# Kernel optimization log

Hardware: AMD Instinct MI355X
Metric: run time of the kernel (lower is better)

Reference implementation:

```python
import jax, jax.numpy as jnp
import numpy as np

BS, L, D = 64, 100, 512
ITEM_NUM = 100000
N = BS * (L + 1)  # number of in-batch candidate items
MASK_VAL = -10000.0


def setup_inputs() -> dict:
    key = jax.random.key(0)
    ks = jax.random.split(key, 8)
    sample_items_id = jax.random.randint(ks[0], (BS, L + 1), 1, ITEM_NUM + 1, dtype=jnp.int32)
    log_mask = jax.random.randint(ks[1], (BS, L), 0, 2, dtype=jnp.int32)
    pop_prob = jax.random.uniform(ks[2], (ITEM_NUM + 1,), minval=1e-3, maxval=1.0, dtype=jnp.float32)
    id_emb = jax.random.normal(ks[3], (ITEM_NUM + 1, D), dtype=jnp.float32) * 0.02
    scale = 1.0 / np.sqrt(D)
    W_ih = jax.random.normal(ks[4], (D, 3 * D), dtype=jnp.float32) * scale
    W_hh = jax.random.normal(ks[5], (D, 3 * D), dtype=jnp.float32) * scale
    b_ih = jnp.zeros((3 * D,), jnp.float32)
    b_hh = jnp.zeros((3 * D,), jnp.float32)
    return dict(sample_items_id=sample_items_id, log_mask=log_mask, pop_prob=pop_prob,
                id_emb=id_emb, W_ih=W_ih, W_hh=W_hh, b_ih=b_ih, b_hh=b_hh)


def gru_forward(x, W_ih, W_hh, b_ih, b_hh):
    # x: (B, T, D) -> per-step hidden states (B, T, D)  (GRU4Rec user encoder)
    B, T, Dh = x.shape
    gates_x = jnp.einsum('btd,de->bte', x, W_ih) + b_ih  # precompute input gates (B,T,3D)

    def step(h, gx):
        gh = h @ W_hh + b_hh
        xr, xz, xn = jnp.split(gx, 3, axis=-1)
        hr, hz, hn = jnp.split(gh, 3, axis=-1)
        r = jax.nn.sigmoid(xr + hr)
        z = jax.nn.sigmoid(xz + hz)
        n = jnp.tanh(xn + r * hn)
        h_new = (1.0 - z) * n + z * h
        return h_new, h_new

    h0 = jnp.zeros((B, Dh), x.dtype)
    _, hs = jax.lax.scan(step, h0, jnp.swapaxes(gates_x, 0, 1))  # (T,B,D)
    return jnp.swapaxes(hs, 0, 1)


def reference(sample_items_id, log_mask, pop_prob, id_emb, W_ih, W_hh, b_ih, b_hh):
    ids_flat = sample_items_id.reshape(-1)                 # (N,)
    debias = jnp.log(pop_prob[ids_flat])                   # (N,) debias_logits
    score_embs = id_emb[ids_flat]                          # (N, D)
    input_embs = score_embs.reshape(BS, L + 1, D)
    prec = gru_forward(input_embs[:, :-1, :], W_ih, W_hh, b_ih, b_hh)  # (BS, L, D)
    prec_vec = prec.reshape(BS * L, D)

    logits = prec_vec @ score_embs.T - debias[None, :]     # (BS*L, N)
    # mask padded candidate columns: cat(log_mask, ones(bs,1)) flattened == 0
    col_valid = jnp.concatenate([log_mask, jnp.ones((BS, 1), log_mask.dtype)], axis=1).reshape(-1)
    logits = jnp.where(col_valid[None, :] == 0, MASK_VAL, logits)
    logits = logits.reshape(BS, L, N)

    # per-sample negative exclusion: column k is rejected for sample i if
    # ids_flat[k] appears anywhere in sample i's own item list
    reject = (ids_flat[None, None, :] == sample_items_id[:, :, None]).any(axis=1)  # (BS, N)
    mask3 = jnp.broadcast_to(reject[:, None, :], (BS, L, N))
    # keep the ground-truth target position (i, j, i*(L+1)+j+1) unmasked
    tgt = jnp.arange(BS)[:, None] * (L + 1) + jnp.arange(L)[None, :] + 1  # (BS, L)
    col = jnp.arange(N)[None, None, :]
    mask3 = mask3 & (col != tgt[:, :, None])
    logits = jnp.where(mask3, MASK_VAL, logits)

    logits = logits.reshape(BS * L, N)
    labels = tgt.reshape(-1)
    logp = jax.nn.log_softmax(logits, axis=-1)
    nll = -jnp.take_along_axis(logp, labels[:, None], axis=1)[:, 0]
    w = (log_mask.reshape(-1) != 0).astype(logits.dtype)
    loss = jnp.sum(nll * w) / jnp.maximum(jnp.sum(w), 1.0)
    return loss
```

## Files before the change

### kernel.cpp

```cpp
#include <hip/hip_runtime.h>
#include <hip/hip_bf16.h>

#define BSZ   64
#define SEQL  100
#define DIM   512
#define L1P   101
#define NCOLS 6464
#define NROWS 6400
#define D3    1536
#define MASKV -10000.0f
#define M0    16.0f

#define SGRP  4
#define SPG   16
#define DBLK  16
#define DPB   32
#define GRU_BLOCKS (SGRP * DBLK)
#define SENT64 0x7FC07FC07FC07FC0ULL
#define INIT_N  409600
#define INIT_NP 410624

typedef __attribute__((ext_vector_type(8))) short bf16x8;
typedef __attribute__((ext_vector_type(4))) float f32x4;

__device__ __forceinline__ float sigm(float x)  { return 1.f / (1.f + __expf(-x)); }
__device__ __forceinline__ float ftanh(float x) { float e = __expf(2.f * x); return 1.f - 2.f / (e + 1.f); }
__device__ __forceinline__ ushort f2bf(float x) {
    __hip_bfloat16 b = __float2bfloat16(x);
    return *(ushort*)&b;
}

__global__ void init_ws(float* s_glob, float* acc, uint4* prec_all)
{
    int t = blockIdx.x * 256 + threadIdx.x;
    if (t < INIT_N) {
        uint4 s; s.x = 0x7FC07FC0u; s.y = 0x7FC07FC0u; s.z = 0x7FC07FC0u; s.w = 0x7FC07FC0u;
        prec_all[t] = s;
    } else if (t < INIT_NP) {
        uint4 z; z.x = 0u; z.y = 0u; z.z = 0u; z.w = 0u;
        prec_all[t] = z;
    }
    if (t < NROWS) s_glob[t] = 0.f;
    if (t < 2) acc[t] = 0.f;
}

__global__ void gather_embs(const int* __restrict__ ids, const float* __restrict__ emb,
                            ushort* __restrict__ score16)
{
    int idx = blockIdx.x * 256 + threadIdx.x;
    int row = idx >> 7, c4 = idx & 127;
    int id = ids[row];
    float4 v = *(const float4*)&emb[(size_t)id * DIM + c4 * 4];
    ushort4 u;
    u.x = f2bf(v.x); u.y = f2bf(v.y); u.z = f2bf(v.z); u.w = f2bf(v.w);
    *(ushort4*)&score16[(size_t)row * DIM + c4 * 4] = u;
}

__global__ void aux_kernel(const int* __restrict__ ids, const float* __restrict__ pop,
                           const int* __restrict__ lmask,
                           float* __restrict__ debias, int* __restrict__ colv)
{
    int k = blockIdx.x * 256 + threadIdx.x;
    if (k >= NCOLS) return;
    int id = ids[k];
    debias[k] = __logf(pop[id]);
    int j = k % L1P;
    colv[k] = (j == SEQL) ? 1 : lmask[(k / L1P) * SEQL + j];
}

__global__ void build_reject(const int* __restrict__ ids, const int* __restrict__ colv,
                             unsigned char* __restrict__ rejm)
{
    __shared__ int s_ids[L1P];
    int i = blockIdx.y;
    int tid = threadIdx.x;
    if (tid < L1P) s_ids[tid] = ids[i * L1P + tid];
    __syncthreads();
    int k = blockIdx.x * 256 + tid;
    if (k >= NCOLS) return;
    int myid = ids[k];
    int rej = 0;
    for (int j = 0; j < L1P; ++j) rej |= (myid == s_ids[j]);
    unsigned char code = (colv[k] == 0) ? 1 : (rej ? 2 : 0);
    rejm[(size_t)i * NCOLS + k] = code;
}

__global__ __launch_bounds__(256) void wt_tile(const float* __restrict__ W,
                                               ushort* __restrict__ WT)
{
    __shared__ float tile[64][65];
    int c0 = blockIdx.x * 64, k0 = blockIdx.y * 64;
    int tx = threadIdx.x & 63, ty = threadIdx.x >> 6;
    for (int r = ty; r < 64; r += 4)
        tile[r][tx] = W[(size_t)(k0 + r) * D3 + c0 + tx];
    __syncthreads();
    for (int r = ty; r < 64; r += 4)
        WT[(size_t)(c0 + r) * DIM + k0 + tx] = f2bf(tile[tx][r]);
}

__global__ __launch_bounds__(256) void gates_mfma(
    const ushort* __restrict__ score16, const ushort* __restrict__ WIT,
    const float* __restrict__ b_ih, float* __restrict__ gates)
{
    int n0 = blockIdx.x * 64, r0 = blockIdx.y * 64;
    int tid = threadIdx.x;
    int w = tid >> 6, lane = tid & 63, l15 = lane & 15, quad = lane >> 4;
    int r = r0 + w * 16 + l15;
    int i = r / SEQL, j = r % SEQL;
    const ushort* ap = score16 + (size_t)(i * L1P + j) * DIM + quad * 8;
    bf16x8 af[16];
#pragma unroll
    for (int c = 0; c < 16; ++c) af[c] = *(const bf16x8*)(ap + c * 32);

    f32x4 acc[4] = {{0,0,0,0},{0,0,0,0},{0,0,0,0},{0,0,0,0}};
#pragma unroll
    for (int c = 0; c < 16; ++c) {
#pragma unroll
        for (int nt = 0; nt < 4; ++nt) {
            const ushort* bp = WIT + (size_t)(n0 + nt * 16 + l15) * DIM + quad * 8 + c * 32;
            bf16x8 bb = *(const bf16x8*)bp;
            acc[nt] = __builtin_amdgcn_mfma_f32_16x16x32_bf16(af[c], bb, acc[nt], 0, 0, 0);
        }
    }
#pragma unroll
    for (int nt = 0; nt < 4; ++nt) {
        int n = n0 + nt * 16 + l15;
        float bi = b_ih[n];
#pragma unroll
        for (int p = 0; p < 4; ++p) {
            int rr = r0 + w * 16 + quad * 4 + p;
            gates[(size_t)rr * D3 + n] = acc[nt][p] + bi;
        }
    }
}

__global__ __launch_bounds__(256) void gru_mfma(
    const ushort* __restrict__ WT,
    const float* __restrict__ b_hh,
    const float* __restrict__ gates,
    ushort* __restrict__ prec16)
{
    __shared__ float  red[2][3][256];
    __shared__ ushort hpub[16][32];

    int b = blockIdx.x;
    int sg = b >> 4, db = b & 15;
    int s0 = sg * SPG, d0 = db * DPB;
    int tid = threadIdx.x;
    int w = tid >> 6, lane = tid & 63, l15 = lane & 15, quad = lane >> 4;
    int wc = w & 1, wk = w >> 1;
    int kb = wk * 8;

    bf16x8 wreg[3][8];
#pragma unroll
    for (int g = 0; g < 3; ++g)
#pragma unroll
        for (int cc = 0; cc < 8; ++cc)
            wreg[g][cc] = *(const bf16x8*)(WT
                + (size_t)(g * 512 + d0 + wc * 16 + l15) * DIM
                + (kb + cc) * 32 + quad * 8);

    int d = d0 + wc * 16 + l15;
    float bhr = b_hh[d], bhz = b_hh[512 + d], bhn = b_hh[1024 + d];
    float hprev[4] = {0.f, 0.f, 0.f, 0.f};

    for (int t = 0; t < SEQL; ++t) {
        float xr[4], xz[4], xn[4];
        if (wk == 0) {
#pragma unroll
            for (int p = 0; p < 4; ++p) {
                int ss = s0 + quad * 4 + p;
                const float* gx = gates + ((size_t)ss * SEQL + t) * D3;
                xr[p] = gx[d]; xz[p] = gx[512 + d]; xn[p] = gx[1024 + d];
            }
        }
        f32x4 acc[3] = {{0,0,0,0},{0,0,0,0},{0,0,0,0}};
        if (t > 0) {
            const ushort* ap = prec16
                + ((size_t)(s0 + l15) * SEQL + (t - 1)) * DIM + quad * 8;
            unsigned long long v[16];
            bool again = true;
            while (again) {
#pragma unroll
                for (int u = 0; u < 16; ++u) {
                    const unsigned long long* p64 = (const unsigned long long*)
                        (ap + (kb + (u >> 1)) * 32 + (u & 1) * 4);
                    v[u] = __hip_atomic_load(p64, __ATOMIC_RELAXED,
                                             __HIP_MEMORY_SCOPE_AGENT);
                }
                unsigned long long bad = 0ull;
#pragma unroll
                for (int u = 0; u < 16; ++u) {
                    unsigned long long x = v[u] ^ SENT64;
                    bad |= (x - 0x0001000100010001ULL) & ~x & 0x8000800080008000ULL;
                }
                again = (bad != 0ull);
                if (again) __builtin_amdgcn_s_sleep(1);
            }
#pragma unroll
            for (int cc = 0; cc < 8; ++cc) {
                union { unsigned long long q[2]; bf16x8 h; } af;
                af.q[0] = v[2 * cc]; af.q[1] = v[2 * cc + 1];
#pragma unroll
                for (int g = 0; g < 3; ++g)
                    acc[g] = __builtin_amdgcn_mfma_f32_16x16x32_bf16(
                        af.h, wreg[g][cc], acc[g], 0, 0, 0);
            }
        }
        if (wk == 1) {
#pragma unroll
            for (int g = 0; g < 3; ++g)
                *(f32x4*)&red[wc][g][lane * 4] = acc[g];
        }
        __syncthreads();
        if (wk == 0) {
#pragma unroll
            for (int p = 0; p < 4; ++p) {
                float a0 = acc[0][p] + red[wc][0][lane * 4 + p];
                float a1 = acc[1][p] + red[wc][1][lane * 4 + p];
                float a2 = acc[2][p] + red[wc][2][lane * 4 + p];
                float r = sigm(xr[p] + a0 + bhr);
                float z = sigm(xz[p] + a1 + bhz);
                float n = ftanh(xn[p] + r * (a2 + bhn));
                float hnew = (1.f - z) * n + z * hprev[p];
                hprev[p] = hnew;
                hpub[quad * 4 + p][wc * 16 + l15] = f2bf(hnew);
            }
        }
        __syncthreads();
        if (tid >= 128) {
            int pt = tid - 128;
            int ss = pt >> 3, gq = pt & 7;
            unsigned long long vv =
                 (unsigned long long)hpub[ss][gq * 4 + 0]
               | ((unsigned long long)hpub[ss][gq * 4 + 1] << 16)
               | ((unsigned long long)hpub[ss][gq * 4 + 2] << 32)
               | ((unsigned long long)hpub[ss][gq * 4 + 3] << 48);
            unsigned long long* dst = (unsigned long long*)
                (prec16 + ((size_t)(s0 + ss) * SEQL + t) * DIM + d0 + gq * 4);
            __hip_atomic_store(dst, vv, __ATOMIC_RELAXED,
                               __HIP_MEMORY_SCOPE_AGENT);
        }
    }
}

__global__ __launch_bounds__(256, 2) void logits_mfma(
    const ushort* __restrict__ prec16, const ushort* __restrict__ score16,
    const float* __restrict__ debias, const unsigned char* __restrict__ rejm,
    float* __restrict__ s_glob, float* __restrict__ label_glob)
{
    __shared__ ushort Bt[2][16 * 512];
    __shared__ float dbs[816];
    __shared__ unsigned char rjs[816];

    int bi = blockIdx.x;
    int i  = bi >> 3;
    int cs = (bi >> 1) & 3;
    int h  = bi & 1;
    int tile0  = cs * 101 + h * 51;
    int ntiles = 51 - h;
    int tid  = threadIdx.x;
    int lane = tid & 63;
    int w    = tid >> 6;
    int l15  = lane & 15, quad = lane >> 4;

    bf16x8 afrag[2][16];
    bool live1 = (w < 3);
    {
        int r0 = i * SEQL + (2 * w) * 16 + l15;
        const ushort* ap = prec16 + (size_t)r0 * DIM + quad * 8;
#pragma unroll
        for (int c = 0; c < 16; ++c) afrag[0][c] = *(const bf16x8*)(ap + c * 32);
    }
    if (live1) {
        int r1 = i * SEQL + (2 * w + 1) * 16 + l15;
        const ushort* ap = prec16 + (size_t)r1 * DIM + quad * 8;
#pragma unroll
        for (int c = 0; c < 16; ++c) afrag[1][c] = *(const bf16x8*)(ap + c * 32);
    }

    int ncols = ntiles * 16;
    int nb0 = tile0 * 16;
    for (int idx = tid; idx < ncols; idx += 256) {
        dbs[idx] = debias[nb0 + idx];
        rjs[idx] = rejm[(size_t)i * NCOLS + nb0 + idx];
    }

    auto stage = [&](int buf, int st) {
        const char* slab = (const char*)(score16 + (size_t)(tile0 + st) * 16 * DIM);
#pragma unroll
        for (int k = 0; k < 4; ++k) {
            int o  = k * 4096 + w * 1024 + lane * 16;
            int so = o ^ (((o >> 10) & 15) << 4);
            __builtin_amdgcn_global_load_lds(
                (const __attribute__((address_space(1))) void*)(slab + so),
                (__attribute__((address_space(3))) void*)((char*)&Bt[buf][0] + k * 4096 + w * 1024),
                16, 0, 0);
        }
    };

    stage(0, 0);
    asm volatile("s_waitcnt vmcnt(0)" ::: "memory");
    __syncthreads();

    float srun0[4] = {0.f, 0.f, 0.f, 0.f};
    float srun1[4] = {0.f, 0.f, 0.f, 0.f};
    int colb = l15 * 1024;
    int q16  = quad * 16;
    int key  = l15 << 4;

    for (int st = 0; st < ntiles; ++st) {
        int cur = st & 1;
        if (st + 1 < ntiles) stage(cur ^ 1, st + 1);

        const char* bt = (const char*)&Bt[cur][0];
        f32x4 acc0[2] = {{0,0,0,0},{0,0,0,0}};
        f32x4 acc1[2] = {{0,0,0,0},{0,0,0,0}};
#pragma unroll
        for (int c = 0; c < 16; ++c) {
            int a = colb + ((c * 64 + q16) ^ key);
            bf16x8 b = *(const bf16x8*)(bt + a);
            acc0[c & 1] = __builtin_amdgcn_mfma_f32_16x16x32_bf16(afrag[0][c], b, acc0[c & 1], 0, 0, 0);
            if (live1)
                acc1[c & 1] = __builtin_amdgcn_mfma_f32_16x16x32_bf16(afrag[1][c], b, acc1[c & 1], 0, 0, 0);
        }

        int mi = st * 16 + l15;
        int n  = nb0 + mi;
        float db = dbs[mi];
        int   mc = rjs[mi];
        int   jj = n - i * L1P - 1;
        {
            int rowb = (2 * w) * 16 + quad * 4;
#pragma unroll
            for (int p = 0; p < 4; ++p) {
                int j = rowb + p;
                float l = acc0[0][p] + acc0[1][p] - db;
                bool is_t = (j == jj);
                bool msk = (mc == 1) || (mc == 2 && !is_t);
                l = msk ? MASKV : l;
                if (is_t && j < SEQL) label_glob[i * SEQL + j] = l;
                if (j < SEQL) srun0[p] += __expf(l - M0);
            }
        }
        if (live1) {
            int rowb = (2 * w + 1) * 16 + quad * 4;
#pragma unroll
            for (int p = 0; p < 4; ++p) {
                int j = rowb + p;
                float l = acc1[0][p] + acc1[1][p] - db;
                bool is_t = (j == jj);
                bool msk = (mc == 1) || (mc == 2 && !is_t);
                l = msk ? MASKV : l;
                if (is_t && j < SEQL) label_glob[i * SEQL + j] = l;
                if (j < SEQL) srun1[p] += __expf(l - M0);
            }
        }
        __syncthreads();
    }

#pragma unroll
    for (int p = 0; p < 4; ++p) {
        float s = srun0[p];
        s += __shfl_xor(s, 1); s += __shfl_xor(s, 2);
        s += __shfl_xor(s, 4); s += __shfl_xor(s, 8);
        if (l15 == 0) {
            int j = (2 * w) * 16 + quad * 4 + p;
            if (j < SEQL) atomicAdd(&s_glob[i * SEQL + j], s);
        }
    }
    if (live1) {
#pragma unroll
        for (int p = 0; p < 4; ++p) {
            float s = srun1[p];
            s += __shfl_xor(s, 1); s += __shfl_xor(s, 2);
            s += __shfl_xor(s, 4); s += __shfl_xor(s, 8);
            if (l15 == 0) {
                int j = (2 * w + 1) * 16 + quad * 4 + p;
                if (j < SEQL) atomicAdd(&s_glob[i * SEQL + j], s);
            }
        }
    }
}

__global__ void nll_reduce(const float* __restrict__ s_glob, const float* __restrict__ label_glob,
                           const int* __restrict__ lmask, float* __restrict__ acc)
{
    int r = blockIdx.x * 256 + threadIdx.x;
    float v = 0.f, wt = 0.f;
    if (r < NROWS) {
        wt = (lmask[r] != 0) ? 1.f : 0.f;
        v  = (M0 + __logf(s_glob[r]) - label_glob[r]) * wt;
    }
#pragma unroll
    for (int o = 32; o; o >>= 1) { v += __shfl_down(v, o); wt += __shfl_down(wt, o); }
    if ((threadIdx.x & 63) == 0) { atomicAdd(&acc[0], v); atomicAdd(&acc[1], wt); }
}

__global__ void finalize(const float* __restrict__ acc, float* __restrict__ out)
{
    out[0] = acc[0] / fmaxf(acc[1], 1.f);
}

extern "C" void kernel_launch(void* const* d_in, const int* in_sizes, int n_in,
                              void* d_out, int out_size, void* d_ws, size_t ws_size,
                              hipStream_t stream)
{
    const int*   ids   = (const int*)d_in[0];
    const int*   lmask = (const int*)d_in[1];
    const float* pop   = (const float*)d_in[2];
    const float* emb   = (const float*)d_in[3];
    const float* W_ih  = (const float*)d_in[4];
    const float* W_hh  = (const float*)d_in[5];
    const float* b_ih  = (const float*)d_in[6];
    const float* b_hh  = (const float*)d_in[7];
    float* out = (float*)d_out;

    ushort* score16 = (ushort*)d_ws;
    ushort* prec16  = score16 + (size_t)NCOLS * DIM;
    ushort* WT      = prec16 + (size_t)(NROWS + 16) * DIM;
    ushort* WIT     = WT + (size_t)D3 * DIM;
    float*  debias  = (float*)(WIT + (size_t)D3 * DIM);
    int*    colv    = (int*)(debias + NCOLS);
    unsigned char* rejm = (unsigned char*)(colv + NCOLS);
    float*  gates   = (float*)(rejm + (size_t)BSZ * NCOLS + 64);
    float*  s_glob  = gates + (size_t)NROWS * D3;
    float*  label_g = s_glob + NROWS;
    float*  acc     = label_g + NROWS;

    init_ws<<<INIT_NP / 256, 256, 0, stream>>>(s_glob, acc, (uint4*)prec16);
    gather_embs<<<(NCOLS * 128) / 256, 256, 0, stream>>>(ids, emb, score16);
    aux_kernel<<<(NCOLS + 255) / 256, 256, 0, stream>>>(ids, pop, lmask, debias, colv);
    build_reject<<<dim3((NCOLS + 255) / 256, BSZ), 256, 0, stream>>>(ids, colv, rejm);
    wt_tile<<<dim3(24, 8), 256, 0, stream>>>(W_hh, WT);
    wt_tile<<<dim3(24, 8), 256, 0, stream>>>(W_ih, WIT);
    gates_mfma<<<dim3(24, 100), 256, 0, stream>>>(score16, WIT, b_ih, gates);
    gru_mfma<<<GRU_BLOCKS, 256, 0, stream>>>(WT, b_hh, gates, prec16);
    logits_mfma<<<BSZ * 8, 256, 0, stream>>>(prec16, score16, debias, rejm, s_glob, label_g);
    nll_reduce<<<(NROWS + 255) / 256, 256, 0, stream>>>(s_glob, label_g, lmask, acc);
    finalize<<<1, 1, 0, stream>>>(acc, out);
}
```

Before: 852.3 us.

## Stage W_ih slab in LDS for gates GEMM and drop GRU publish barrier

The gates GEMM now loads each block's 64-column W_ih slab into swizzled LDS once with global_load_lds and reuses it across ten 64-row tiles, double-buffering the A-fragment register loads. This cuts the launch from 2400 to 240 blocks. The GRU step kernel now packs bf16 hidden values with lane shuffles and stores them to global directly from the compute waves. That removes the LDS staging buffer and one __syncthreads per timestep, and the reduction buffer is double-buffered by step parity to avoid a race. The costs are fewer blocks and lower occupancy for the gates kernel (64KB of LDS per block), and narrower 8-byte stores issued from fewer lanes.

```diff
diff --git a/kernel.cpp b/kernel.cpp
--- a/kernel.cpp
+++ b/kernel.cpp
@@ -98,39 +98,74 @@
         WT[(size_t)(c0 + r) * DIM + k0 + tx] = f2bf(tile[tx][r]);
 }
 
-__global__ __launch_bounds__(256) void gates_mfma(
+__global__ __launch_bounds__(256, 1) void gates_mfma(
     const ushort* __restrict__ score16, const ushort* __restrict__ WIT,
     const float* __restrict__ b_ih, float* __restrict__ gates)
 {
-    int n0 = blockIdx.x * 64, r0 = blockIdx.y * 64;
+    __shared__ ushort Bs[64 * 512];
+    int n0 = blockIdx.x * 64;
+    int rowbase = blockIdx.y * 640;
     int tid = threadIdx.x;
     int w = tid >> 6, lane = tid & 63, l15 = lane & 15, quad = lane >> 4;
-    int r = r0 + w * 16 + l15;
-    int i = r / SEQL, j = r % SEQL;
-    const ushort* ap = score16 + (size_t)(i * L1P + j) * DIM + quad * 8;
-    bf16x8 af[16];
-#pragma unroll
-    for (int c = 0; c < 16; ++c) af[c] = *(const bf16x8*)(ap + c * 32);
-
-    f32x4 acc[4] = {{0,0,0,0},{0,0,0,0},{0,0,0,0},{0,0,0,0}};
-#pragma unroll
-    for (int c = 0; c < 16; ++c) {
+
+    {
+        const char* slab = (const char*)(WIT + (size_t)n0 * DIM);
+#pragma unroll
+        for (int k = 0; k < 16; ++k) {
+            int o  = k * 4096 + w * 1024 + lane * 16;
+            int so = o ^ (((o >> 10) & 15) << 4);
+            __builtin_amdgcn_global_load_lds(
+                (const __attribute__((address_space(1))) void*)(slab + so),
+                (__attribute__((address_space(3))) void*)((char*)Bs + k * 4096 + w * 1024),
+                16, 0, 0);
+        }
+    }
+    float bi[4];
+#pragma unroll
+    for (int nt = 0; nt < 4; ++nt) bi[nt] = b_ih[n0 + nt * 16 + l15];
+
+    asm volatile("s_waitcnt vmcnt(0)" ::: "memory");
+    __syncthreads();
+
+    int key = l15 << 4;
+    bf16x8 afA[16], afB[16];
+
+    auto load_af = [&](bf16x8 (&dst)[16], int rt) {
+        int r = rowbase + rt * 64 + w * 16 + l15;
+        int i = r / SEQL, j = r - i * SEQL;
+        const ushort* ap = score16 + (size_t)(i * L1P + j) * DIM + quad * 8;
+#pragma unroll
+        for (int c = 0; c < 16; ++c) dst[c] = *(const bf16x8*)(ap + c * 32);
+    };
+    auto do_tile = [&](const bf16x8 (&af)[16], int rt) {
+        f32x4 acc[4] = {{0,0,0,0},{0,0,0,0},{0,0,0,0},{0,0,0,0}};
+        const char* bt = (const char*)Bs;
+#pragma unroll
+        for (int c = 0; c < 16; ++c) {
+#pragma unroll
+            for (int nt = 0; nt < 4; ++nt) {
+                int a = (nt * 16 + l15) * 1024 + ((c * 64 + quad * 16) ^ key);
+                bf16x8 bb = *(const bf16x8*)(bt + a);
+                acc[nt] = __builtin_amdgcn_mfma_f32_16x16x32_bf16(af[c], bb, acc[nt], 0, 0, 0);
+            }
+        }
 #pragma unroll
         for (int nt = 0; nt < 4; ++nt) {
-            const ushort* bp = WIT + (size_t)(n0 + nt * 16 + l15) * DIM + quad * 8 + c * 32;
-            bf16x8 bb = *(const bf16x8*)bp;
-            acc[nt] = __builtin_amdgcn_mfma_f32_16x16x32_bf16(af[c], bb, acc[nt], 0, 0, 0);
-        }
-    }
-#pragma unroll
-    for (int nt = 0; nt < 4; ++nt) {
-        int n = n0 + nt * 16 + l15;
-        float bi = b_ih[n];
-#pragma unroll
-        for (int p = 0; p < 4; ++p) {
-            int rr = r0 + w * 16 + quad * 4 + p;
-            gates[(size_t)rr * D3 + n] = acc[nt][p] + bi;
-        }
+#pragma unroll
+            for (int p = 0; p < 4; ++p) {
+                int rr = rowbase + rt * 64 + w * 16 + quad * 4 + p;
+                gates[(size_t)rr * D3 + n0 + nt * 16 + l15] = acc[nt][p] + bi[nt];
+            }
+        }
+    };
+
+    load_af(afA, 0);
+#pragma unroll
+    for (int rp = 0; rp < 5; ++rp) {
+        load_af(afB, rp * 2 + 1);
+        do_tile(afA, rp * 2);
+        if (rp < 4) load_af(afA, rp * 2 + 2);
+        do_tile(afB, rp * 2 + 1);
     }
 }
 
@@ -140,8 +175,7 @@
     const float* __restrict__ gates,
     ushort* __restrict__ prec16)
 {
-    __shared__ float  red[2][3][256];
-    __shared__ ushort hpub[16][32];
+    __shared__ float red[2][2][3][256];
 
     int b = blockIdx.x;
     int sg = b >> 4, db = b & 15;
@@ -165,6 +199,7 @@
     float hprev[4] = {0.f, 0.f, 0.f, 0.f};
 
     for (int t = 0; t < SEQL; ++t) {
+        int tp = t & 1;
         float xr[4], xz[4], xn[4];
         if (wk == 0) {
 #pragma unroll
@@ -210,36 +245,32 @@
         if (wk == 1) {
 #pragma unroll
             for (int g = 0; g < 3; ++g)
-                *(f32x4*)&red[wc][g][lane * 4] = acc[g];
+                *(f32x4*)&red[tp][wc][g][lane * 4] = acc[g];
         }
         __syncthreads();
         if (wk == 0) {
 #pragma unroll
             for (int p = 0; p < 4; ++p) {
-                float a0 = acc[0][p] + red[wc][0][lane * 4 + p];
-                float a1 = acc[1][p] + red[wc][1][lane * 4 + p];
-                float a2 = acc[2][p] + red[wc][2][lane * 4 + p];
+                float a0 = acc[0][p] + red[tp][wc][0][lane * 4 + p];
+                float a1 = acc[1][p] + red[tp][wc][1][lane * 4 + p];
+                float a2 = acc[2][p] + red[tp][wc][2][lane * 4 + p];
                 float r = sigm(xr[p] + a0 + bhr);
                 float z = sigm(xz[p] + a1 + bhz);
                 float n = ftanh(xn[p] + r * (a2 + bhn));
                 float hnew = (1.f - z) * n + z * hprev[p];
                 hprev[p] = hnew;
-                hpub[quad * 4 + p][wc * 16 + l15] = f2bf(hnew);
-            }
-        }
-        __syncthreads();
-        if (tid >= 128) {
-            int pt = tid - 128;
-            int ss = pt >> 3, gq = pt & 7;
-            unsigned long long vv =
-                 (unsigned long long)hpub[ss][gq * 4 + 0]
-               | ((unsigned long long)hpub[ss][gq * 4 + 1] << 16)
-               | ((unsigned long long)hpub[ss][gq * 4 + 2] << 32)
-               | ((unsigned long long)hpub[ss][gq * 4 + 3] << 48);
-            unsigned long long* dst = (unsigned long long*)
-                (prec16 + ((size_t)(s0 + ss) * SEQL + t) * DIM + d0 + gq * 4);
-            __hip_atomic_store(dst, vv, __ATOMIC_RELAXED,
-                               __HIP_MEMORY_SCOPE_AGENT);
+                unsigned b16 = f2bf(hnew);
+                unsigned lo = b16 | (((unsigned)__shfl_xor((int)b16, 1)) << 16);
+                unsigned long long hi = (unsigned)__shfl_xor((int)lo, 2);
+                unsigned long long vv = (unsigned long long)lo | (hi << 32);
+                if ((l15 & 3) == 0) {
+                    unsigned long long* dst = (unsigned long long*)
+                        (prec16 + ((size_t)(s0 + quad * 4 + p) * SEQL + t) * DIM
+                         + d0 + wc * 16 + l15);
+                    __hip_atomic_store(dst, vv, __ATOMIC_RELAXED,
+                                       __HIP_MEMORY_SCOPE_AGENT);
+                }
+            }
         }
     }
 }
@@ -434,7 +465,7 @@
     build_reject<<<dim3((NCOLS + 255) / 256, BSZ), 256, 0, stream>>>(ids, colv, rejm);
     wt_tile<<<dim3(24, 8), 256, 0, stream>>>(W_hh, WT);
     wt_tile<<<dim3(24, 8), 256, 0, stream>>>(W_ih, WIT);
-    gates_mfma<<<dim3(24, 100), 256, 0, stream>>>(score16, WIT, b_ih, gates);
+    gates_mfma<<<dim3(24, 10), 256, 0, stream>>>(score16, WIT, b_ih, gates);
     gru_mfma<<<GRU_BLOCKS, 256, 0, stream>>>(WT, b_hh, gates, prec16);
     logits_mfma<<<BSZ * 8, 256, 0, stream>>>(prec16, score16, debias, rejm, s_glob, label_g);
     nll_reduce<<<(NROWS + 255) / 256, 256, 0, stream>>>(s_glob, label_g, lmask, acc);
```

Result: slower. 911.6 us (+7.0%).
